# Performance work log

Measured on AMD Instinct MI355X. Metric: run time of the kernel, lower is better.

## Reference

```python
import jax, jax.numpy as jnp
import numpy as np

N_NODES = 50000
N_EDGES = 800000
N_NF = 16
N_EF = 8
HID = 300
MSG = 128
N_HIDDEN = 300
N_PRED = 8
N_GRAPHS = 64


def _lin_init(key, fan_in, fan_out):
    kw, kb = jax.random.split(key)
    lim = 1.0 / np.sqrt(fan_in)
    w = jax.random.uniform(kw, (fan_in, fan_out), minval=-lim, maxval=lim, dtype=jnp.float32)
    b = jax.random.uniform(kb, (fan_out,), minval=-lim, maxval=lim, dtype=jnp.float32)
    return w, b


def setup_inputs() -> dict:
    key = jax.random.key(0)
    ks = jax.random.split(key, 16)
    x = jax.random.normal(ks[0], (N_NODES, N_NF), dtype=jnp.float32)
    edge_index = jax.random.randint(ks[1], (2, N_EDGES), 0, N_NODES, dtype=jnp.int32)
    edge_attr = jax.random.normal(ks[2], (N_EDGES, N_EF), dtype=jnp.float32)
    batch = jnp.sort(jax.random.randint(ks[3], (N_NODES,), 0, N_GRAPHS, dtype=jnp.int32))
    # message MLP: (2*n_nf+n_ef) -> 300 -> 300 -> 300 -> msg_dim
    mw1, mb1 = _lin_init(ks[4], 2 * N_NF + N_EF, HID)
    mw2, mb2 = _lin_init(ks[5], HID, HID)
    mw3, mb3 = _lin_init(ks[6], HID, HID)
    mw4, mb4 = _lin_init(ks[7], HID, MSG)
    # node MLP: msg_dim -> 300 -> 300 -> 300 -> n_hidden
    nw1, nb1 = _lin_init(ks[8], MSG, HID)
    nw2, nb2 = _lin_init(ks[9], HID, HID)
    nw3, nb3 = _lin_init(ks[10], HID, HID)
    nw4, nb4 = _lin_init(ks[11], HID, N_HIDDEN)
    # final linear: n_hidden -> n_predict
    lw, lb = _lin_init(ks[12], N_HIDDEN, N_PRED)
    return {
        "x": x, "edge_index": edge_index, "edge_attr": edge_attr, "batch": batch,
        "mw1": mw1, "mb1": mb1, "mw2": mw2, "mb2": mb2, "mw3": mw3, "mb3": mb3,
        "mw4": mw4, "mb4": mb4,
        "nw1": nw1, "nb1": nb1, "nw2": nw2, "nb2": nb2, "nw3": nw3, "nb3": nb3,
        "nw4": nw4, "nb4": nb4, "lw": lw, "lb": lb,
    }


def reference(x, edge_index, edge_attr, batch,
              mw1, mb1, mw2, mb2, mw3, mb3, mw4, mb4,
              nw1, nb1, nw2, nb2, nw3, nb3, nw4, nb4, lw, lb):
    src = edge_index[0]  # x_j (source, PyG flow source_to_target)
    dst = edge_index[1]  # x_i (target), also scatter destination
    # message: cat([x_i, x_j, e_ij]) -> MLP
    tmp = jnp.concatenate([x[dst], x[src], edge_attr], axis=1)  # [E, 2*n_nf+n_ef]
    h = jax.nn.relu(tmp @ mw1 + mb1)
    h = jax.nn.relu(h @ mw2 + mb2)
    h = jax.nn.relu(h @ mw3 + mb3)
    msg = h @ mw4 + mb4  # [E, msg_dim]
    # aggregate: scatter-add into target nodes
    aggr = jax.ops.segment_sum(msg, dst, num_segments=N_NODES)  # [N, msg_dim]
    # update: node MLP
    h = jax.nn.relu(aggr @ nw1 + nb1)
    h = jax.nn.relu(h @ nw2 + nb2)
    h = jax.nn.relu(h @ nw3 + nb3)
    node = h @ nw4 + nb4  # [N, n_hidden]
    # global mean pool over graphs
    sums = jax.ops.segment_sum(node, batch, num_segments=N_GRAPHS)
    counts = jax.ops.segment_sum(jnp.ones((node.shape[0],), node.dtype), batch, num_segments=N_GRAPHS)
    pooled = sums / jnp.maximum(counts, 1.0)[:, None]  # [G, n_hidden]
    # dropout(p=0.5, training=self.training) is identity in eval mode
    return pooled @ lw + lb  # [G, n_predict]
```

## Files before the change

kernel.cpp:

```cpp
#include <hip/hip_runtime.h>
#include <hip/hip_bf16.h>
#include <stdint.h>

#define E_TOTAL 800000
#define NNODES  50000
#define NGRAPHS 64
#define NPRED   8
#define MPAD    50048
#define EBLK    12500
#define NBLK    782

#define TILE_B  20480
#define SCR_B   40960
#define LDSZ    (2*TILE_B + SCR_B)

typedef short v8s __attribute__((ext_vector_type(8)));
typedef float v4f __attribute__((ext_vector_type(4)));
typedef float f4  __attribute__((ext_vector_type(4)));

__device__ __forceinline__ void gload_lds16(const void* g, void* l) {
    __builtin_amdgcn_global_load_lds(
        (const __attribute__((address_space(1))) uint32_t*)g,
        (__attribute__((address_space(3))) uint32_t*)l, 16, 0, 0);
}

__device__ __forceinline__ short f2bf_s(float f) {
    __hip_bfloat16 h = __float2bfloat16(f);
    return *reinterpret_cast<short*>(&h);
}

template <bool EDGE>
__global__ __launch_bounds__(256, 2)
void chain_kernel(const float* __restrict__ x, const int* __restrict__ ei,
                  const float* __restrict__ ea,
                  const __hip_bfloat16* __restrict__ aggrb,
                  const char* __restrict__ wimg,
                  const float* __restrict__ b1, const float* __restrict__ b2,
                  const float* __restrict__ b3, const float* __restrict__ b4,
                  float* __restrict__ outp)
{
    __shared__ __align__(16) char lds[LDSZ];
    const int tid  = threadIdx.x;
    const int lane = tid & 63;
    const int wc   = tid >> 6;
    const int l15  = lane & 15;
    const int kk   = lane >> 4;
    char* scr = lds + 2*TILE_B;
    const int rowbase = blockIdx.x*64;

    constexpr int KT1 = EDGE ? 2 : 4;
    constexpr int T   = KT1 + 30;

    auto stagef = [&](int t, int slot_){
        const char* s = wimg + (size_t)t*TILE_B + (size_t)tid*16;
        char* d = lds + slot_*TILE_B + wc*1024;
#pragma unroll
        for (int i = 0; i < 5; ++i) gload_lds16(s + i*4096, d + i*4096);
    };

    v4f acc[4][5];
#pragma unroll
    for (int p = 0; p < 4; ++p)
#pragma unroll
        for (int n = 0; n < 5; ++n) acc[p][n] = (v4f){0.f,0.f,0.f,0.f};

    float bb1[5], bb2[5], bb3[5], bb4[5];
#pragma unroll
    for (int n = 0; n < 5; ++n) {
        int colb = wc*80 + n*16 + l15;
        bb1[n] = b1[colb]; bb2[n] = b2[colb]; bb3[n] = b3[colb];
        if (EDGE) bb4[n] = (n < 2) ? b4[wc*32 + n*16 + l15] : 0.f;
        else      bb4[n] = b4[colb];
    }

    v8s af1[KT1][4];
    if (EDGE) {
#pragma unroll
        for (int p = 0; p < 4; ++p) {
            const int e = rowbase + p*16 + l15;
            const int nidx = (kk < 2) ? ei[E_TOTAL + e] : ei[e];
            const float* xs = x + (size_t)nidx*16 + (kk & 1)*8;
            f4 p0 = *(const f4*)xs, p1 = *(const f4*)(xs + 4);
            v8s a0, a1;
#pragma unroll
            for (int j = 0; j < 4; ++j) { a0[j] = f2bf_s(p0[j]); a0[4+j] = f2bf_s(p1[j]); }
            if (kk == 0) {
                const float* es = ea + (size_t)e*8;
                f4 q0 = *(const f4*)es, q1 = *(const f4*)(es + 4);
#pragma unroll
                for (int j = 0; j < 4; ++j) { a1[j] = f2bf_s(q0[j]); a1[4+j] = f2bf_s(q1[j]); }
            } else {
#pragma unroll
                for (int j = 0; j < 8; ++j) a1[j] = 0;
            }
            af1[0][p] = a0; af1[1][p] = a1;
        }
    } else {
#pragma unroll
        for (int p = 0; p < 4; ++p) {
            const int grow = rowbase + p*16 + l15;
#pragma unroll
            for (int kt = 0; kt < KT1; ++kt)
                af1[kt][p] = *(const v8s*)((const char*)aggrb +
                    (size_t)grow*256 + kt*64 + kk*16);
        }
    }

    stagef(0, 0);
    int tt = 0, slot = 0;

#define TILE_BEGIN()                                                            \
    { asm volatile("s_waitcnt vmcnt(0)" ::: "memory");                          \
      __builtin_amdgcn_s_barrier();                                             \
      if (tt + 1 < T) stagef(tt + 1, slot ^ 1); }

#define TILE_END()  { ++tt; slot ^= 1; }

#define MFMA_TILE(AF_, NT_, CB_)                                                \
    { const char* sl_ = lds + slot*TILE_B;                                      \
      _Pragma("unroll")                                                         \
      for (int n_ = 0; n_ < NT_; ++n_) {                                        \
        int r_ = (CB_) + n_*16 + l15;                                           \
        int ch_ = (kk | ((r_&1)<<2)) ^ ((r_>>1)&7);                             \
        v8s b_ = *(const v8s*)(sl_ + (r_>>1)*128 + (ch_<<4));                   \
        _Pragma("unroll")                                                       \
        for (int p_ = 0; p_ < 4; ++p_)                                          \
          acc[p_][n_] = __builtin_amdgcn_mfma_f32_16x16x32_bf16(                \
              (AF_)[p_], b_, acc[p_][n_], 0, 0, 0);                             \
      } }

#define LOAD_AFRAG(KT_, A_)                                                     \
    { _Pragma("unroll")                                                         \
      for (int p_ = 0; p_ < 4; ++p_) {                                          \
        int c_ = ((KT_)*4 + kk) ^ (l15 & 7);                                    \
        (A_)[p_] = *(const v8s*)(scr + (p_*16 + l15)*640 + (c_<<4));            \
      } }

#define DUMP_RELU(BB_)                                                          \
    { __builtin_amdgcn_s_barrier();        \
      _Pragma("unroll")                                                         \
      for (int p_ = 0; p_ < 4; ++p_)                                            \
        _Pragma("unroll")                                                       \
        for (int n_ = 0; n_ < 5; ++n_) {                                        \
          int col_ = wc*80 + n_*16 + l15;                                       \
          _Pragma("unroll")                                                     \
          for (int rr_ = 0; rr_ < 4; ++rr_) {                                   \
            int row_ = p_*16 + kk*4 + rr_;                                      \
            float v_ = fmaxf(acc[p_][n_][rr_] + (BB_)[n_], 0.f);                \
            *(__hip_bfloat16*)(scr + row_*640 +                                 \
                (((col_>>3) ^ (row_&7))<<4) + (col_&7)*2) = __float2bfloat16(v_); \
          }                                                                     \
          acc[p_][n_] = (v4f){0.f,0.f,0.f,0.f};                                 \
        }                                                                       \
      asm volatile("s_waitcnt lgkmcnt(0)" ::: "memory"); }

#pragma unroll
    for (int kt = 0; kt < KT1; ++kt) { TILE_BEGIN(); MFMA_TILE(af1[kt], 5, wc*80); TILE_END(); }
    DUMP_RELU(bb1);
#pragma unroll
    for (int kt = 0; kt < 10; ++kt) {
        TILE_BEGIN(); v8s A_[4]; LOAD_AFRAG(kt, A_); MFMA_TILE(A_, 5, wc*80); TILE_END();
    }
    DUMP_RELU(bb2);
#pragma unroll
    for (int kt = 0; kt < 10; ++kt) {
        TILE_BEGIN(); v8s A_[4]; LOAD_AFRAG(kt, A_); MFMA_TILE(A_, 5, wc*80); TILE_END();
    }
    DUMP_RELU(bb3);
    if (EDGE) {
#pragma unroll
        for (int kt = 0; kt < 10; ++kt) {
            TILE_BEGIN(); v8s A_[4]; LOAD_AFRAG(kt, A_); MFMA_TILE(A_, 2, wc*32); TILE_END();
        }
#pragma unroll
        for (int p = 0; p < 4; ++p) {
#pragma unroll
            for (int rr = 0; rr < 4; ++rr) {
                int erow = rowbase + p*16 + kk*4 + rr;
                int d = ei[E_TOTAL + erow];
                float* ag = outp + (size_t)d*128;
#pragma unroll
                for (int n = 0; n < 2; ++n) {
                    int col = wc*32 + n*16 + l15;
                    atomicAdd(ag + col, acc[p][n][rr] + bb4[n]);
                }
            }
        }
    } else {
#pragma unroll
        for (int kt = 0; kt < 10; ++kt) {
            TILE_BEGIN(); v8s A_[4]; LOAD_AFRAG(kt, A_); MFMA_TILE(A_, 5, wc*80); TILE_END();
        }
#pragma unroll
        for (int p = 0; p < 4; ++p) {
#pragma unroll
            for (int n = 0; n < 5; ++n) {
                int col = wc*80 + n*16 + l15;
#pragma unroll
                for (int rr = 0; rr < 4; ++rr) {
                    int grow = rowbase + p*16 + kk*4 + rr;
                    outp[(size_t)grow*320 + col] = acc[p][n][rr] + bb4[n];
                }
            }
        }
    }
#undef TILE_BEGIN
#undef TILE_END
#undef MFMA_TILE
#undef LOAD_AFRAG
#undef DUMP_RELU
}

__global__ void repack_tiles(const float* __restrict__ src, char* __restrict__ img,
                             int K, int N, int KT)
{
    int t = blockIdx.x*256 + threadIdx.x;
    if (t >= KT*10240) return;
    int tile = t / 10240;
    int rem  = t - tile*10240;
    int r    = rem >> 5;
    int k32  = rem & 31;
    int c4   = k32 >> 3;
    int j    = k32 & 7;
    int kg   = tile*32 + k32;
    float v = (r < N && kg < K) ? src[(size_t)kg*N + r] : 0.f;
    int ch = (c4 | ((r&1)<<2)) ^ ((r>>1)&7);
    size_t addr = (size_t)tile*TILE_B + (size_t)(r>>1)*128 + (ch<<4) + j*2;
    *(__hip_bfloat16*)(img + addr) = __float2bfloat16(v);
}

__global__ void pad_bias(const float* __restrict__ src, float* __restrict__ dst,
                         int N, int Npad)
{
    int t = blockIdx.x*256 + threadIdx.x;
    if (t < Npad) dst[t] = (t < N) ? src[t] : 0.f;
}

__global__ void cvt_aggr(const float* __restrict__ aggr, __hip_bfloat16* __restrict__ out)
{
    int t = blockIdx.x*256 + threadIdx.x;
    int row = t >> 7;
    float v = (row < NNODES) ? aggr[t] : 0.f;
    out[t] = __float2bfloat16(v);
}

__global__ void graph_starts_kernel(const int* __restrict__ batch,
                                    int* __restrict__ starts)
{
    int g = threadIdx.x;
    if (g > NGRAPHS) return;
    int lo = 0, hi = NNODES;
    while (lo < hi) {
        int mid = (lo + hi) >> 1;
        if (batch[mid] < g) lo = mid + 1; else hi = mid;
    }
    starts[g] = lo;
}

__global__ void pool_kernel(const float* __restrict__ node,
                            const int* __restrict__ starts,
                            float* __restrict__ pooled)
{
    __shared__ float red[8][32];
    int g   = blockIdx.x;
    int col = blockIdx.y*32 + (threadIdx.x & 31);
    int rl  = threadIdx.x >> 5;
    int s = starts[g], e = starts[g + 1];
    float sum = 0.f;
    if (col < 300)
        for (int i = s + rl; i < e; i += 8) sum += node[(size_t)i*320 + col];
    red[rl][threadIdx.x & 31] = sum;
    __syncthreads();
    if (rl == 0 && col < 300) {
        float tot = 0.f;
#pragma unroll
        for (int r = 0; r < 8; ++r) tot += red[r][threadIdx.x & 31];
        float cnt = (float)(e - s);
        pooled[g*300 + col] = tot / fmaxf(cnt, 1.0f);
    }
}

__global__ void final_kernel(const float* __restrict__ pooled,
                             const float* __restrict__ lw,
                             const float* __restrict__ lb,
                             float* __restrict__ out)
{
    int t = threadIdx.x;
    int g = t / NPRED, p = t % NPRED;
    float s = lb[p];
    for (int k = 0; k < 300; ++k)
        s = fmaf(pooled[g*300 + k], lw[k*NPRED + p], s);
    out[g*NPRED + p] = s;
}

extern "C" void kernel_launch(void* const* d_in, const int* in_sizes, int n_in,
                              void* d_out, int out_size, void* d_ws, size_t ws_size,
                              hipStream_t stream)
{
    const float* x     = (const float*)d_in[0];
    const int*   ei    = (const int*)d_in[1];
    const float* ea    = (const float*)d_in[2];
    const int*   batch = (const int*)d_in[3];
    const float* mw[4] = {(const float*)d_in[4], (const float*)d_in[6],
                          (const float*)d_in[8], (const float*)d_in[10]};
    const float* mb[4] = {(const float*)d_in[5], (const float*)d_in[7],
                          (const float*)d_in[9], (const float*)d_in[11]};
    const float* nw[4] = {(const float*)d_in[12], (const float*)d_in[14],
                          (const float*)d_in[16], (const float*)d_in[18]};
    const float* nb[4] = {(const float*)d_in[13], (const float*)d_in[15],
                          (const float*)d_in[17], (const float*)d_in[19]};
    const float* lw = (const float*)d_in[20];
    const float* lb = (const float*)d_in[21];
    float* out = (float*)d_out;

    char* ws = (char*)d_ws;
    size_t off = 0;
    auto alloc = [&](size_t bytes) -> void* {
        void* p = ws + off;
        off += (bytes + 255) & ~(size_t)255;
        return p;
    };

    float*          aggr   = (float*)alloc((size_t)MPAD*128*4);
    __hip_bfloat16* aggrb  = (__hip_bfloat16*)alloc((size_t)MPAD*128*2);
    float*          node   = (float*)alloc((size_t)MPAD*320*4);
    char*           wimg_e = (char*)alloc((size_t)32*TILE_B);
    char*           wimg_n = (char*)alloc((size_t)34*TILE_B);
    float* mbp[4]; float* nbp[4];
    for (int i = 0; i < 4; ++i) { mbp[i] = (float*)alloc(320*4); nbp[i] = (float*)alloc(320*4); }
    float* pooled = (float*)alloc(64*300*4);
    int*   starts = (int*)alloc(65*4);

    const int mK[4]  = {40, 300, 300, 300},  mN[4]  = {300, 300, 300, 128};
    const int nK[4]  = {128, 300, 300, 300}, nN[4]  = {300, 300, 300, 300};
    const int mKT[4] = {2, 10, 10, 10},      nKT[4] = {4, 10, 10, 10};
    {
        size_t te = 0, tn = 0;
        for (int i = 0; i < 4; ++i) {
            repack_tiles<<<mKT[i]*40, 256, 0, stream>>>(mw[i], wimg_e + te*TILE_B,
                                                        mK[i], mN[i], mKT[i]);
            te += mKT[i];
            repack_tiles<<<nKT[i]*40, 256, 0, stream>>>(nw[i], wimg_n + tn*TILE_B,
                                                        nK[i], nN[i], nKT[i]);
            tn += nKT[i];
            pad_bias<<<2, 256, 0, stream>>>(mb[i], mbp[i], mN[i], 320);
            pad_bias<<<2, 256, 0, stream>>>(nb[i], nbp[i], nN[i], 320);
        }
    }
    hipMemsetAsync(aggr, 0, (size_t)NNODES*128*4, stream);
    graph_starts_kernel<<<1, 128, 0, stream>>>(batch, starts);

    chain_kernel<true><<<EBLK, 256, 0, stream>>>(
        x, ei, ea, nullptr, wimg_e, mbp[0], mbp[1], mbp[2], mbp[3], aggr);

    cvt_aggr<<<(MPAD*128)/256, 256, 0, stream>>>(aggr, aggrb);
    chain_kernel<false><<<NBLK, 256, 0, stream>>>(
        x, ei, ea, aggrb, wimg_n, nbp[0], nbp[1], nbp[2], nbp[3], node);

    pool_kernel<<<dim3(64, 10), 256, 0, stream>>>(node, starts, pooled);
    final_kernel<<<1, 512, 0, stream>>>(pooled, lw, lb, out);
}
```

Measured before the change: 872.7 us.

## Load MFMA weight fragments directly from global memory instead of staging via LDS

Drops the double-buffered LDS staging of weight tiles and reads B fragments straight from a simpler row-major repacked weight image in global memory, register double-buffered. Only the activation scratch stays in LDS. This frees LDS so occupancy can rise to three blocks per CU and removes most per-tile barriers. The node kernel now converts fp32 aggregates to bf16 on the fly, which removes the separate cvt_aggr kernel. In exchange, weight reads now depend on L1/L2 hit rates, are less coalesced, and use more registers.

```diff
diff --git a/kernel.cpp b/kernel.cpp
--- a/kernel.cpp
+++ b/kernel.cpp
@@ -10,53 +10,43 @@
 #define EBLK    12500
 #define NBLK    782
 
-#define TILE_B  20480
 #define SCR_B   40960
-#define LDSZ    (2*TILE_B + SCR_B)
+
+#define E_L1 0
+#define E_L2 40960
+#define E_L3 245760
+#define E_L4 450560
+#define N_L1 0
+#define N_L2 81920
+#define N_L3 286720
+#define N_L4 491520
 
 typedef short v8s __attribute__((ext_vector_type(8)));
 typedef float v4f __attribute__((ext_vector_type(4)));
 typedef float f4  __attribute__((ext_vector_type(4)));
 
-__device__ __forceinline__ void gload_lds16(const void* g, void* l) {
-    __builtin_amdgcn_global_load_lds(
-        (const __attribute__((address_space(1))) uint32_t*)g,
-        (__attribute__((address_space(3))) uint32_t*)l, 16, 0, 0);
-}
-
 __device__ __forceinline__ short f2bf_s(float f) {
     __hip_bfloat16 h = __float2bfloat16(f);
     return *reinterpret_cast<short*>(&h);
 }
 
 template <bool EDGE>
-__global__ __launch_bounds__(256, 2)
+__global__ __launch_bounds__(256, 3)
 void chain_kernel(const float* __restrict__ x, const int* __restrict__ ei,
                   const float* __restrict__ ea,
-                  const __hip_bfloat16* __restrict__ aggrb,
+                  const float* __restrict__ aggr_in,
                   const char* __restrict__ wimg,
                   const float* __restrict__ b1, const float* __restrict__ b2,
                   const float* __restrict__ b3, const float* __restrict__ b4,
                   float* __restrict__ outp)
 {
-    __shared__ __align__(16) char lds[LDSZ];
+    __shared__ __align__(16) char scr[SCR_B];
     const int tid  = threadIdx.x;
     const int lane = tid & 63;
     const int wc   = tid >> 6;
     const int l15  = lane & 15;
     const int kk   = lane >> 4;
-    char* scr = lds + 2*TILE_B;
     const int rowbase = blockIdx.x*64;
-
-    constexpr int KT1 = EDGE ? 2 : 4;
-    constexpr int T   = KT1 + 30;
-
-    auto stagef = [&](int t, int slot_){
-        const char* s = wimg + (size_t)t*TILE_B + (size_t)tid*16;
-        char* d = lds + slot_*TILE_B + wc*1024;
-#pragma unroll
-        for (int i = 0; i < 5; ++i) gload_lds16(s + i*4096, d + i*4096);
-    };
 
     v4f acc[4][5];
 #pragma unroll
@@ -73,71 +63,40 @@
         else      bb4[n] = b4[colb];
     }
 
-    v8s af1[KT1][4];
-    if (EDGE) {
-#pragma unroll
-        for (int p = 0; p < 4; ++p) {
-            const int e = rowbase + p*16 + l15;
-            const int nidx = (kk < 2) ? ei[E_TOTAL + e] : ei[e];
-            const float* xs = x + (size_t)nidx*16 + (kk & 1)*8;
-            f4 p0 = *(const f4*)xs, p1 = *(const f4*)(xs + 4);
-            v8s a0, a1;
-#pragma unroll
-            for (int j = 0; j < 4; ++j) { a0[j] = f2bf_s(p0[j]); a0[4+j] = f2bf_s(p1[j]); }
-            if (kk == 0) {
-                const float* es = ea + (size_t)e*8;
-                f4 q0 = *(const f4*)es, q1 = *(const f4*)(es + 4);
-#pragma unroll
-                for (int j = 0; j < 4; ++j) { a1[j] = f2bf_s(q0[j]); a1[4+j] = f2bf_s(q1[j]); }
-            } else {
-#pragma unroll
-                for (int j = 0; j < 8; ++j) a1[j] = 0;
-            }
-            af1[0][p] = a0; af1[1][p] = a1;
-        }
-    } else {
-#pragma unroll
-        for (int p = 0; p < 4; ++p) {
-            const int grow = rowbase + p*16 + l15;
-#pragma unroll
-            for (int kt = 0; kt < KT1; ++kt)
-                af1[kt][p] = *(const v8s*)((const char*)aggrb +
-                    (size_t)grow*256 + kt*64 + kk*16);
-        }
-    }
-
-    stagef(0, 0);
-    int tt = 0, slot = 0;
-
-#define TILE_BEGIN()                                                            \
-    { asm volatile("s_waitcnt vmcnt(0)" ::: "memory");                          \
-      __builtin_amdgcn_s_barrier();                                             \
-      if (tt + 1 < T) stagef(tt + 1, slot ^ 1); }
-
-#define TILE_END()  { ++tt; slot ^= 1; }
-
-#define MFMA_TILE(AF_, NT_, CB_)                                                \
-    { const char* sl_ = lds + slot*TILE_B;                                      \
+#define BLOAD(DST, BASE, STRIDE, T, CB, NT)                                     \
+    { const char* bp_ = (BASE) + (size_t)(T)*(STRIDE);                          \
       _Pragma("unroll")                                                         \
-      for (int n_ = 0; n_ < NT_; ++n_) {                                        \
-        int r_ = (CB_) + n_*16 + l15;                                           \
-        int ch_ = (kk | ((r_&1)<<2)) ^ ((r_>>1)&7);                             \
-        v8s b_ = *(const v8s*)(sl_ + (r_>>1)*128 + (ch_<<4));                   \
+      for (int n_ = 0; n_ < (NT); ++n_)                                         \
+        (DST)[n_] = *(const v8s*)(bp_ + ((CB)+n_*16+l15)*64 + kk*16); }
+
+#define ALOAD(DST, KT)                                                          \
+    { _Pragma("unroll")                                                         \
+      for (int p_ = 0; p_ < 4; ++p_) {                                          \
+        int c_ = ((KT)*4 + kk) ^ (l15 & 7);                                     \
+        (DST)[p_] = *(const v8s*)(scr + (p_*16 + l15)*640 + (c_<<4)); } }
+
+#define AGLOAD(DST, KT)                                                         \
+    { _Pragma("unroll")                                                         \
+      for (int p_ = 0; p_ < 4; ++p_) {                                          \
+        const float* ap_ = aggr_in + (size_t)(rowbase+p_*16+l15)*128            \
+                            + (KT)*32 + kk*8;                                   \
+        f4 u0_ = *(const f4*)ap_, u1_ = *(const f4*)(ap_+4);                    \
+        v8s t_;                                                                 \
+        _Pragma("unroll")                                                       \
+        for (int j_ = 0; j_ < 4; ++j_) { t_[j_] = f2bf_s(u0_[j_]);              \
+                                         t_[4+j_] = f2bf_s(u1_[j_]); }          \
+        (DST)[p_] = t_; } }
+
+#define MFMA_NT(A_, B_, NT)                                                     \
+    { _Pragma("unroll")                                                         \
+      for (int n_ = 0; n_ < (NT); ++n_)                                         \
         _Pragma("unroll")                                                       \
         for (int p_ = 0; p_ < 4; ++p_)                                          \
           acc[p_][n_] = __builtin_amdgcn_mfma_f32_16x16x32_bf16(                \
-              (AF_)[p_], b_, acc[p_][n_], 0, 0, 0);                             \
-      } }
-
-#define LOAD_AFRAG(KT_, A_)                                                     \
-    { _Pragma("unroll")                                                         \
-      for (int p_ = 0; p_ < 4; ++p_) {                                          \
-        int c_ = ((KT_)*4 + kk) ^ (l15 & 7);                                    \
-        (A_)[p_] = *(const v8s*)(scr + (p_*16 + l15)*640 + (c_<<4));            \
-      } }
+              (A_)[p_], (B_)[n_], acc[p_][n_], 0, 0, 0); }
 
 #define DUMP_RELU(BB_)                                                          \
-    { __builtin_amdgcn_s_barrier();        \
+    { __builtin_amdgcn_s_barrier();         \
       _Pragma("unroll")                                                         \
       for (int p_ = 0; p_ < 4; ++p_)                                            \
         _Pragma("unroll")                                                       \
@@ -152,25 +111,112 @@
           }                                                                     \
           acc[p_][n_] = (v4f){0.f,0.f,0.f,0.f};                                 \
         }                                                                       \
-      asm volatile("s_waitcnt lgkmcnt(0)" ::: "memory"); }
-
-#pragma unroll
-    for (int kt = 0; kt < KT1; ++kt) { TILE_BEGIN(); MFMA_TILE(af1[kt], 5, wc*80); TILE_END(); }
+      asm volatile("s_waitcnt lgkmcnt(0)" ::: "memory");                        \
+      __builtin_amdgcn_s_barrier(); }
+
+    if (EDGE) {
+        v8s af1[2][4];
+#pragma unroll
+        for (int p = 0; p < 4; ++p) {
+            const int e = rowbase + p*16 + l15;
+            const int nidx = (kk < 2) ? ei[E_TOTAL + e] : ei[e];
+            const float* xs = x + (size_t)nidx*16 + (kk & 1)*8;
+            f4 p0 = *(const f4*)xs, p1 = *(const f4*)(xs + 4);
+            v8s a0, a1;
+#pragma unroll
+            for (int j = 0; j < 4; ++j) { a0[j] = f2bf_s(p0[j]); a0[4+j] = f2bf_s(p1[j]); }
+            if (kk == 0) {
+                const float* es = ea + (size_t)e*8;
+                f4 q0 = *(const f4*)es, q1 = *(const f4*)(es + 4);
+#pragma unroll
+                for (int j = 0; j < 4; ++j) { a1[j] = f2bf_s(q0[j]); a1[4+j] = f2bf_s(q1[j]); }
+            } else {
+#pragma unroll
+                for (int j = 0; j < 8; ++j) a1[j] = 0;
+            }
+            af1[0][p] = a0; af1[1][p] = a1;
+        }
+        v8s Bc[5], Bn[5];
+        BLOAD(Bc, wimg + E_L1, 20480, 0, wc*80, 5);
+#pragma unroll
+        for (int kt = 0; kt < 2; ++kt) {
+            if (kt < 1) BLOAD(Bn, wimg + E_L1, 20480, kt+1, wc*80, 5);
+            MFMA_NT(af1[kt], Bc, 5);
+            if (kt < 1) {
+#pragma unroll
+                for (int q = 0; q < 5; ++q) Bc[q] = Bn[q];
+            }
+        }
+    } else {
+        v8s Ac[4], An[4], Bc[5], Bn[5];
+        AGLOAD(Ac, 0);
+        BLOAD(Bc, wimg + N_L1, 20480, 0, wc*80, 5);
+#pragma unroll
+        for (int kt = 0; kt < 4; ++kt) {
+            if (kt < 3) { AGLOAD(An, kt+1); BLOAD(Bn, wimg + N_L1, 20480, kt+1, wc*80, 5); }
+            MFMA_NT(Ac, Bc, 5);
+            if (kt < 3) {
+#pragma unroll
+                for (int q = 0; q < 4; ++q) Ac[q] = An[q];
+#pragma unroll
+                for (int q = 0; q < 5; ++q) Bc[q] = Bn[q];
+            }
+        }
+    }
     DUMP_RELU(bb1);
-#pragma unroll
-    for (int kt = 0; kt < 10; ++kt) {
-        TILE_BEGIN(); v8s A_[4]; LOAD_AFRAG(kt, A_); MFMA_TILE(A_, 5, wc*80); TILE_END();
+
+    {
+        const char* wb = wimg + (EDGE ? E_L2 : N_L2);
+        v8s Ac[4], An[4], Bc[5], Bn[5];
+        ALOAD(Ac, 0);
+        BLOAD(Bc, wb, 20480, 0, wc*80, 5);
+#pragma unroll
+        for (int kt = 0; kt < 10; ++kt) {
+            if (kt < 9) { ALOAD(An, kt+1); BLOAD(Bn, wb, 20480, kt+1, wc*80, 5); }
+            MFMA_NT(Ac, Bc, 5);
+            if (kt < 9) {
+#pragma unroll
+                for (int q = 0; q < 4; ++q) Ac[q] = An[q];
+#pragma unroll
+                for (int q = 0; q < 5; ++q) Bc[q] = Bn[q];
+            }
+        }
     }
     DUMP_RELU(bb2);
-#pragma unroll
-    for (int kt = 0; kt < 10; ++kt) {
-        TILE_BEGIN(); v8s A_[4]; LOAD_AFRAG(kt, A_); MFMA_TILE(A_, 5, wc*80); TILE_END();
+
+    {
+        const char* wb = wimg + (EDGE ? E_L3 : N_L3);
+        v8s Ac[4], An[4], Bc[5], Bn[5];
+        ALOAD(Ac, 0);
+        BLOAD(Bc, wb, 20480, 0, wc*80, 5);
+#pragma unroll
+        for (int kt = 0; kt < 10; ++kt) {
+            if (kt < 9) { ALOAD(An, kt+1); BLOAD(Bn, wb, 20480, kt+1, wc*80, 5); }
+            MFMA_NT(Ac, Bc, 5);
+            if (kt < 9) {
+#pragma unroll
+                for (int q = 0; q < 4; ++q) Ac[q] = An[q];
+#pragma unroll
+                for (int q = 0; q < 5; ++q) Bc[q] = Bn[q];
+            }
+        }
     }
     DUMP_RELU(bb3);
+
     if (EDGE) {
+        v8s Ac[4], An[4], Bc[2], Bn[2];
+        ALOAD(Ac, 0);
+        BLOAD(Bc, wimg + E_L4, 8192, 0, wc*32, 2);
 #pragma unroll
         for (int kt = 0; kt < 10; ++kt) {
-            TILE_BEGIN(); v8s A_[4]; LOAD_AFRAG(kt, A_); MFMA_TILE(A_, 2, wc*32); TILE_END();
+            if (kt < 9) { ALOAD(An, kt+1); BLOAD(Bn, wimg + E_L4, 8192, kt+1, wc*32, 2); }
+            MFMA_NT(Ac, Bc, 2);
+            if (kt < 9) {
+#pragma unroll
+                for (int q = 0; q < 4; ++q) Ac[q] = An[q];
+#pragma unroll
+                for (int q = 0; q < 2; ++q) Bc[q] = Bn[q];
+            }
         }
 #pragma unroll
         for (int p = 0; p < 4; ++p) {
@@ -187,9 +233,19 @@
             }
         }
     } else {
+        v8s Ac[4], An[4], Bc[5], Bn[5];
+        ALOAD(Ac, 0);
+        BLOAD(Bc, wimg + N_L4, 20480, 0, wc*80, 5);
 #pragma unroll
         for (int kt = 0; kt < 10; ++kt) {
-            TILE_BEGIN(); v8s A_[4]; LOAD_AFRAG(kt, A_); MFMA_TILE(A_, 5, wc*80); TILE_END();
+            if (kt < 9) { ALOAD(An, kt+1); BLOAD(Bn, wimg + N_L4, 20480, kt+1, wc*80, 5); }
+            MFMA_NT(Ac, Bc, 5);
+            if (kt < 9) {
+#pragma unroll
+                for (int q = 0; q < 4; ++q) Ac[q] = An[q];
+#pragma unroll
+                for (int q = 0; q < 5; ++q) Bc[q] = Bn[q];
+            }
         }
 #pragma unroll
         for (int p = 0; p < 4; ++p) {
@@ -204,29 +260,25 @@
             }
         }
     }
-#undef TILE_BEGIN
-#undef TILE_END
-#undef MFMA_TILE
-#undef LOAD_AFRAG
+#undef BLOAD
+#undef ALOAD
+#undef AGLOAD
+#undef MFMA_NT
 #undef DUMP_RELU
 }
 
 __global__ void repack_tiles(const float* __restrict__ src, char* __restrict__ img,
-                             int K, int N, int KT)
+                             int K, int N, int KT, int ROWS)
 {
     int t = blockIdx.x*256 + threadIdx.x;
-    if (t >= KT*10240) return;
-    int tile = t / 10240;
-    int rem  = t - tile*10240;
-    int r    = rem >> 5;
-    int k32  = rem & 31;
-    int c4   = k32 >> 3;
-    int j    = k32 & 7;
+    if (t >= KT*ROWS*32) return;
+    int k32  = t & 31;
+    int r    = (t >> 5) % ROWS;
+    int tile = t / (ROWS*32);
     int kg   = tile*32 + k32;
     float v = (r < N && kg < K) ? src[(size_t)kg*N + r] : 0.f;
-    int ch = (c4 | ((r&1)<<2)) ^ ((r>>1)&7);
-    size_t addr = (size_t)tile*TILE_B + (size_t)(r>>1)*128 + (ch<<4) + j*2;
-    *(__hip_bfloat16*)(img + addr) = __float2bfloat16(v);
+    *(__hip_bfloat16*)(img + (size_t)tile*ROWS*64 + (size_t)r*64 + k32*2) =
+        __float2bfloat16(v);
 }
 
 __global__ void pad_bias(const float* __restrict__ src, float* __restrict__ dst,
@@ -234,14 +286,6 @@
 {
     int t = blockIdx.x*256 + threadIdx.x;
     if (t < Npad) dst[t] = (t < N) ? src[t] : 0.f;
-}
-
-__global__ void cvt_aggr(const float* __restrict__ aggr, __hip_bfloat16* __restrict__ out)
-{
-    int t = blockIdx.x*256 + threadIdx.x;
-    int row = t >> 7;
-    float v = (row < NNODES) ? aggr[t] : 0.f;
-    out[t] = __float2bfloat16(v);
 }
 
 __global__ void graph_starts_kernel(const int* __restrict__ batch,
@@ -321,41 +365,38 @@
         return p;
     };
 
-    float*          aggr   = (float*)alloc((size_t)MPAD*128*4);
-    __hip_bfloat16* aggrb  = (__hip_bfloat16*)alloc((size_t)MPAD*128*2);
-    float*          node   = (float*)alloc((size_t)MPAD*320*4);
-    char*           wimg_e = (char*)alloc((size_t)32*TILE_B);
-    char*           wimg_n = (char*)alloc((size_t)34*TILE_B);
+    float* aggr   = (float*)alloc((size_t)MPAD*128*4);
+    float* node   = (float*)alloc((size_t)MPAD*320*4);
+    char*  wimg_e = (char*)alloc(532480);
+    char*  wimg_n = (char*)alloc(696320);
     float* mbp[4]; float* nbp[4];
     for (int i = 0; i < 4; ++i) { mbp[i] = (float*)alloc(320*4); nbp[i] = (float*)alloc(320*4); }
     float* pooled = (float*)alloc(64*300*4);
     int*   starts = (int*)alloc(65*4);
 
-    const int mK[4]  = {40, 300, 300, 300},  mN[4]  = {300, 300, 300, 128};
-    const int nK[4]  = {128, 300, 300, 300}, nN[4]  = {300, 300, 300, 300};
-    const int mKT[4] = {2, 10, 10, 10},      nKT[4] = {4, 10, 10, 10};
-    {
-        size_t te = 0, tn = 0;
-        for (int i = 0; i < 4; ++i) {
-            repack_tiles<<<mKT[i]*40, 256, 0, stream>>>(mw[i], wimg_e + te*TILE_B,
-                                                        mK[i], mN[i], mKT[i]);
-            te += mKT[i];
-            repack_tiles<<<nKT[i]*40, 256, 0, stream>>>(nw[i], wimg_n + tn*TILE_B,
-                                                        nK[i], nN[i], nKT[i]);
-            tn += nKT[i];
-            pad_bias<<<2, 256, 0, stream>>>(mb[i], mbp[i], mN[i], 320);
-            pad_bias<<<2, 256, 0, stream>>>(nb[i], nbp[i], nN[i], 320);
-        }
-    }
-    hipMemsetAsync(aggr, 0, (size_t)NNODES*128*4, stream);
+    auto rp = [&](const float* srcw, char* dst, int K, int N, int KT, int ROWS) {
+        repack_tiles<<<(KT*ROWS*32 + 255)/256, 256, 0, stream>>>(srcw, dst, K, N, KT, ROWS);
+    };
+    rp(mw[0], wimg_e + E_L1,  40, 300,  2, 320);
+    rp(mw[1], wimg_e + E_L2, 300, 300, 10, 320);
+    rp(mw[2], wimg_e + E_L3, 300, 300, 10, 320);
+    rp(mw[3], wimg_e + E_L4, 300, 128, 10, 128);
+    rp(nw[0], wimg_n + N_L1, 128, 300,  4, 320);
+    rp(nw[1], wimg_n + N_L2, 300, 300, 10, 320);
+    rp(nw[2], wimg_n + N_L3, 300, 300, 10, 320);
+    rp(nw[3], wimg_n + N_L4, 300, 300, 10, 320);
+    for (int i = 0; i < 4; ++i) {
+        pad_bias<<<2, 256, 0, stream>>>(mb[i], mbp[i], (i==3)?128:300, 320);
+        pad_bias<<<2, 256, 0, stream>>>(nb[i], nbp[i], 300, 320);
+    }
+    hipMemsetAsync(aggr, 0, (size_t)MPAD*128*4, stream);
     graph_starts_kernel<<<1, 128, 0, stream>>>(batch, starts);
 
     chain_kernel<true><<<EBLK, 256, 0, stream>>>(
         x, ei, ea, nullptr, wimg_e, mbp[0], mbp[1], mbp[2], mbp[3], aggr);
 
-    cvt_aggr<<<(MPAD*128)/256, 256, 0, stream>>>(aggr, aggrb);
     chain_kernel<false><<<NBLK, 256, 0, stream>>>(
-        x, ei, ea, aggrb, wimg_n, nbp[0], nbp[1], nbp[2], nbp[3], node);
+        x, ei, ea, aggr, wimg_n, nbp[0], nbp[1], nbp[2], nbp[3], node);
 
     pool_kernel<<<dim3(64, 10), 256, 0, stream>>>(node, starts, pooled);
     final_kernel<<<1, 512, 0, stream>>>(pooled, lw, lb, out);
```

New measurement: 1.507 ms. +72.6%, slower.
